# Kernel optimization log

Measured on AMD Instinct MI355X. Metric: run time of the kernel, lower is better.

Reference implementation:

```python
import jax, jax.numpy as jnp
import numpy as np

MAX_WORDS = 128  # static word capacity (stands in for dynamic max_word_num)


def setup_inputs() -> dict:
    key = jax.random.key(0)
    k1, k2 = jax.random.split(key)
    L, B, D = 512, 256, 256
    char_feats = jax.random.normal(k1, (L, B, D), dtype=jnp.float32)
    # sorted random word ids, densified so each row's ids are contiguous 0..n-1
    raw = jnp.sort(jax.random.randint(k2, (B, L), 0, MAX_WORDS), axis=1)
    bump = jnp.concatenate(
        [jnp.zeros((B, 1), jnp.int32), (raw[:, 1:] != raw[:, :-1]).astype(jnp.int32)],
        axis=1,
    )
    word_ids = jnp.cumsum(bump, axis=1)  # [B, L], non-decreasing, < MAX_WORDS
    attention_mask = jnp.ones((B, L), dtype=jnp.int32)
    return {"char_feats": char_feats, "word_ids": word_ids, "attention_mask": attention_mask}


def _pool(char_feats, word_ids, attention_mask):
    # char_feats: [L, B, D] time-major; word_ids/attention_mask: [B, L]
    L, B, D = char_feats.shape
    char_nums = jnp.sum(attention_mask, axis=1) - 2  # drop [CLS]/[SEP]
    pos = jnp.arange(L)
    # chars at positions 1 .. char_nums (inclusive) participate, per torch slicing
    valid = (pos[None, :] >= 1) & (pos[None, :] < 1 + char_nums[:, None])  # [B, L]
    seg = jnp.where(valid, word_ids, MAX_WORDS)  # overflow bucket for invalid chars
    feats_bld = jnp.transpose(char_feats, (1, 0, 2))  # [B, L, D]

    seg_sum = jax.vmap(
        lambda s, f: jax.ops.segment_sum(f, s, num_segments=MAX_WORDS + 1)
    )(seg, feats_bld)[:, :MAX_WORDS]  # [B, W, D]
    counts = jax.vmap(
        lambda s: jax.ops.segment_sum(jnp.ones((L,), jnp.float32), s, num_segments=MAX_WORDS + 1)
    )(seg)[:, :MAX_WORDS]  # [B, W]

    word_nums = jnp.max(word_ids, axis=1) + 1  # [B]
    masks = jnp.arange(MAX_WORDS)[:, None] < word_nums[None, :]  # [W, B]
    means = seg_sum / jnp.maximum(counts, 1.0)[..., None]  # counts>=1 within word_num
    word_feats = jnp.where(masks.T[..., None], means, 0.0)  # zero padded word slots
    return jnp.transpose(word_feats, (1, 0, 2)), masks  # [W, B, D], [W, B]


def reference(char_feats, word_ids, attention_mask):
    return _pool(char_feats, word_ids, attention_mask)
```

## Files before the change

kernel.cpp:

```cpp
#include <hip/hip_runtime.h>
#include <hip/hip_bf16.h>

#define LSEQ 512
#define BATCH 256
#define DIM 256
#define WMAX 128
#define WPB 16
#define BLOCKS_PER_B (WMAX / WPB)
#define ROW4 (BATCH * DIM / 4)
#define BD4 (DIM / 4)

__global__ __launch_bounds__(256) void word_pool_kernel(
    const float* __restrict__ feats,
    const int* __restrict__ word_ids,
    const int* __restrict__ amask,
    float* __restrict__ out)
{
    const int b = blockIdx.x >> 3;
    const int wbase = (blockIdx.x & 7) * WPB;
    const int t = threadIdx.x;

    __shared__ int sids[LSEQ];
    __shared__ int scount[WMAX];
    __shared__ int scum[WMAX];
    __shared__ int sstart[WMAX];
    __shared__ int s_masksum;

    if (t == 0) s_masksum = 0;
    if (t < WMAX) scount[t] = 0;
    __syncthreads();

    int msum = 0;
    for (int p = t; p < LSEQ; p += 256) {
        sids[p] = word_ids[b * LSEQ + p];
        msum += amask[b * LSEQ + p];
    }
    atomicAdd(&s_masksum, msum);
    __syncthreads();

    const int char_num = s_masksum - 2;
    const int word_num = sids[LSEQ - 1] + 1;
    int pend = 1 + char_num;
    if (pend > LSEQ) pend = LSEQ;

    for (int p = 1 + t; p < pend; p += 256) {
        atomicAdd(&scount[sids[p]], 1);
    }
    __syncthreads();

    if (t < WMAX) scum[t] = scount[t];
    __syncthreads();
    #pragma unroll
    for (int off = 1; off < WMAX; off <<= 1) {
        int add = 0;
        if (t < WMAX && t >= off) add = scum[t - off];
        __syncthreads();
        if (t < WMAX) scum[t] += add;
        __syncthreads();
    }
    if (t < WMAX) sstart[t] = 1 + (t > 0 ? scum[t - 1] : 0);
    __syncthreads();

    const int lane = t & 63;
    const int wi = t >> 6;
    const float4* __restrict__ f4 = (const float4*)feats;
    float4* __restrict__ o4 = (float4*)out;
    const int boff = b * BD4 + lane;

    for (int w = wbase + wi; w < wbase + WPB; w += 4) {
        const int c = scount[w];
        const int base = sstart[w];
        float4 acc = make_float4(0.f, 0.f, 0.f, 0.f);
        #pragma unroll 4
        for (int i = 0; i < c; i++) {
            float4 v = f4[(size_t)(base + i) * ROW4 + boff];
            acc.x += v.x; acc.y += v.y; acc.z += v.z; acc.w += v.w;
        }
        const float inv = 1.0f / (float)(c > 0 ? c : 1);
        float4 val = make_float4(acc.x * inv, acc.y * inv, acc.z * inv, acc.w * inv);
        o4[(size_t)w * ROW4 + boff] = val;
    }

    if (wbase == 0 && t < WMAX) {
        out[(size_t)WMAX * BATCH * DIM + (size_t)t * BATCH + b] =
            (t < word_num) ? 1.0f : 0.0f;
    }
}

extern "C" void kernel_launch(void* const* d_in, const int* in_sizes, int n_in,
                              void* d_out, int out_size, void* d_ws, size_t ws_size,
                              hipStream_t stream) {
    const float* char_feats = (const float*)d_in[0];
    const int* word_ids     = (const int*)d_in[1];
    const int* amask        = (const int*)d_in[2];
    float* out              = (float*)d_out;

    word_pool_kernel<<<BATCH * BLOCKS_PER_B, 256, 0, stream>>>(
        char_feats, word_ids, amask, out);
}
```

Before: 210.4 us.

## Balance word pooling by splitting character positions evenly across wavefronts

Instead of assigning a fixed 16 words per block and 4 words per wavefront, each block takes an equal slice of character positions and each wavefront a quarter of it. The wavefront then streams its rows and emits a word's mean whenever a boundary is crossed, so load balance no longer depends on word lengths. Word start positions now come from boundary detection on sorted ids, replacing the atomic histogram and shared-memory scan. Loads are software-pipelined in groups of four rows, and the id and mask reads use int4 plus a shuffle reduction. The trade-off is more complex control flow, with data-dependent branches inside the inner loop.

```diff
diff --git a/kernel.cpp b/kernel.cpp
--- a/kernel.cpp
+++ b/kernel.cpp
@@ -5,8 +5,7 @@
 #define BATCH 256
 #define DIM 256
 #define WMAX 128
-#define WPB 16
-#define BLOCKS_PER_B (WMAX / WPB)
+#define NCHUNK 8
 #define ROW4 (BATCH * DIM / 4)
 #define BD4 (DIM / 4)
 
@@ -17,71 +16,112 @@
     float* __restrict__ out)
 {
     const int b = blockIdx.x >> 3;
-    const int wbase = (blockIdx.x & 7) * WPB;
+    const int chunk = blockIdx.x & 7;
     const int t = threadIdx.x;
+    const int lane = t & 63;
+    const int wi = t >> 6;
 
     __shared__ int sids[LSEQ];
-    __shared__ int scount[WMAX];
-    __shared__ int scum[WMAX];
-    __shared__ int sstart[WMAX];
-    __shared__ int s_masksum;
+    __shared__ int sstart[WMAX + 1];
+    __shared__ int spart[4];
 
-    if (t == 0) s_masksum = 0;
-    if (t < WMAX) scount[t] = 0;
+    int msum = 0;
+    if (t < 128) {
+        int4 q = ((const int4*)(word_ids + b * LSEQ))[t];
+        ((int4*)sids)[t] = q;
+    } else {
+        int4 m = ((const int4*)(amask + b * LSEQ))[t - 128];
+        msum = m.x + m.y + m.z + m.w;
+    }
+    #pragma unroll
+    for (int off = 32; off; off >>= 1) msum += __shfl_down(msum, off, 64);
+    if (lane == 0) spart[wi] = msum;
     __syncthreads();
 
-    int msum = 0;
-    for (int p = t; p < LSEQ; p += 256) {
-        sids[p] = word_ids[b * LSEQ + p];
-        msum += amask[b * LSEQ + p];
-    }
-    atomicAdd(&s_masksum, msum);
+    const int char_num = spart[0] + spart[1] + spart[2] + spart[3] - 2;
+    int pend = 1 + char_num;
+    if (pend < 1) pend = 1;
+    if (pend > LSEQ) pend = LSEQ;
+
+    if (t <= WMAX) sstart[t] = pend;
     __syncthreads();
 
-    const int char_num = s_masksum - 2;
-    const int word_num = sids[LSEQ - 1] + 1;
-    int pend = 1 + char_num;
-    if (pend > LSEQ) pend = LSEQ;
-
     for (int p = 1 + t; p < pend; p += 256) {
-        atomicAdd(&scount[sids[p]], 1);
+        if (p == 1 || sids[p] != sids[p - 1]) sstart[sids[p]] = p;
     }
+    if (t == 0) sstart[0] = 1;
     __syncthreads();
 
-    if (t < WMAX) scum[t] = scount[t];
-    __syncthreads();
-    #pragma unroll
-    for (int off = 1; off < WMAX; off <<= 1) {
-        int add = 0;
-        if (t < WMAX && t >= off) add = scum[t - off];
-        __syncthreads();
-        if (t < WMAX) scum[t] += add;
-        __syncthreads();
-    }
-    if (t < WMAX) sstart[t] = 1 + (t > 0 ? scum[t - 1] : 0);
-    __syncthreads();
+    auto word_at = [&](int pos) -> int {
+        if (pos >= pend) return sids[pend - 1] + 1;
+        int w = sids[pos];
+        return (sstart[w] >= pos) ? w : w + 1;
+    };
 
-    const int lane = t & 63;
-    const int wi = t >> 6;
+    const int pend1 = pend - 1;
+    const int P0 = 1 + (chunk * pend1) / NCHUNK;
+    const int P1 = 1 + ((chunk + 1) * pend1) / NCHUNK;
+    const int span = P1 - P0;
+    const int Q0 = P0 + (wi * span) / 4;
+    const int Q1 = P0 + ((wi + 1) * span) / 4;
+
+    int w0 = (chunk == 0 && wi == 0) ? 0 : word_at(Q0);
+    int w1 = (chunk == NCHUNK - 1 && wi == 3) ? WMAX : word_at(Q1);
+
     const float4* __restrict__ f4 = (const float4*)feats;
     float4* __restrict__ o4 = (float4*)out;
     const int boff = b * BD4 + lane;
 
-    for (int w = wbase + wi; w < wbase + WPB; w += 4) {
-        const int c = scount[w];
-        const int base = sstart[w];
-        float4 acc = make_float4(0.f, 0.f, 0.f, 0.f);
-        #pragma unroll 4
-        for (int i = 0; i < c; i++) {
-            float4 v = f4[(size_t)(base + i) * ROW4 + boff];
+    const int p_lo = sstart[w0];
+    const int p_hi = sstart[w1];
+
+    int cur = w0;
+    int nxt = (cur < w1) ? sstart[cur + 1] : 0;
+    float4 acc = make_float4(0.f, 0.f, 0.f, 0.f);
+    int p = p_lo;
+
+    auto ldrow = [&](int r) -> float4 {
+        int rr = r < p_hi ? r : p_hi - 1;
+        return f4[(size_t)rr * ROW4 + boff];
+    };
+
+    float4 va0, va1, va2, va3;
+    if (p < p_hi) { va0 = ldrow(p); va1 = ldrow(p+1); va2 = ldrow(p+2); va3 = ldrow(p+3); }
+
+    while (p < p_hi) {
+        float4 vb0, vb1, vb2, vb3;
+        if (p + 4 < p_hi) { vb0 = ldrow(p+4); vb1 = ldrow(p+5); vb2 = ldrow(p+6); vb3 = ldrow(p+7); }
+        #pragma unroll
+        for (int j = 0; j < 4; j++) {
+            int pp = p + j;
+            if (pp >= p_hi) break;
+            while (pp >= nxt) {
+                int c = nxt - sstart[cur];
+                float inv = 1.0f / (float)(c > 0 ? c : 1);
+                o4[(size_t)cur * ROW4 + boff] =
+                    make_float4(acc.x * inv, acc.y * inv, acc.z * inv, acc.w * inv);
+                acc = make_float4(0.f, 0.f, 0.f, 0.f);
+                cur++;
+                nxt = sstart[cur + 1];
+            }
+            float4 v = (j == 0) ? va0 : (j == 1) ? va1 : (j == 2) ? va2 : va3;
             acc.x += v.x; acc.y += v.y; acc.z += v.z; acc.w += v.w;
         }
-        const float inv = 1.0f / (float)(c > 0 ? c : 1);
-        float4 val = make_float4(acc.x * inv, acc.y * inv, acc.z * inv, acc.w * inv);
-        o4[(size_t)w * ROW4 + boff] = val;
+        va0 = vb0; va1 = vb1; va2 = vb2; va3 = vb3;
+        p += 4;
     }
 
-    if (wbase == 0 && t < WMAX) {
+    while (cur < w1) {
+        int c = sstart[cur + 1] - sstart[cur];
+        float inv = 1.0f / (float)(c > 0 ? c : 1);
+        o4[(size_t)cur * ROW4 + boff] =
+            make_float4(acc.x * inv, acc.y * inv, acc.z * inv, acc.w * inv);
+        acc = make_float4(0.f, 0.f, 0.f, 0.f);
+        cur++;
+    }
+
+    if (chunk == 0 && t < WMAX) {
+        int word_num = sids[LSEQ - 1] + 1;
         out[(size_t)WMAX * BATCH * DIM + (size_t)t * BATCH + b] =
             (t < word_num) ? 1.0f : 0.0f;
     }
@@ -95,6 +135,6 @@
     const int* amask        = (const int*)d_in[2];
     float* out              = (float*)d_out;
 
-    word_pool_kernel<<<BATCH * BLOCKS_PER_B, 256, 0, stream>>>(
+    word_pool_kernel<<<BATCH * NCHUNK, 256, 0, stream>>>(
         char_feats, word_ids, amask, out);
 }
```

Result: no change. 207.9 us (-1.2%).

## Split segment metadata into separate kernel and batch feature loads in pool kernel

Applied to the files above, without the earlier changes.

Moves the per-batch word-boundary computation into a small meta kernel that finds segment starts by detecting id changes, replacing the atomic histogram and prefix scan. Word starts go to workspace, and a separate pool kernel gives each wavefront one word and issues up to eight loads at once before accumulating. The aim is to drop the metadata work that each of the eight blocks per batch repeated, and to raise memory-level parallelism in the reduction. The cost is a second launch and a round trip through workspace memory.

```diff
diff --git a/kernel.cpp b/kernel.cpp
--- a/kernel.cpp
+++ b/kernel.cpp
@@ -5,86 +5,99 @@
 #define BATCH 256
 #define DIM 256
 #define WMAX 128
-#define WPB 16
-#define BLOCKS_PER_B (WMAX / WPB)
 #define ROW4 (BATCH * DIM / 4)
 #define BD4 (DIM / 4)
+#define MSTRIDE (WMAX + 2)
 
-__global__ __launch_bounds__(256) void word_pool_kernel(
-    const float* __restrict__ feats,
+__global__ __launch_bounds__(256) void meta_kernel(
     const int* __restrict__ word_ids,
     const int* __restrict__ amask,
+    int* __restrict__ meta,
     float* __restrict__ out)
 {
-    const int b = blockIdx.x >> 3;
-    const int wbase = (blockIdx.x & 7) * WPB;
+    const int b = blockIdx.x;
     const int t = threadIdx.x;
+    const int lane = t & 63;
+    const int wi = t >> 6;
 
     __shared__ int sids[LSEQ];
-    __shared__ int scount[WMAX];
-    __shared__ int scum[WMAX];
-    __shared__ int sstart[WMAX];
-    __shared__ int s_masksum;
+    __shared__ int spart[4];
+    __shared__ int sstart[WMAX + 1];
 
-    if (t == 0) s_masksum = 0;
-    if (t < WMAX) scount[t] = 0;
+    int msum = 0;
+    if (t < 128) {
+        ((int4*)sids)[t] = ((const int4*)(word_ids + b * LSEQ))[t];
+    } else {
+        int4 m = ((const int4*)(amask + b * LSEQ))[t - 128];
+        msum = m.x + m.y + m.z + m.w;
+    }
+    #pragma unroll
+    for (int off = 32; off; off >>= 1) msum += __shfl_down(msum, off, 64);
+    if (lane == 0) spart[wi] = msum;
     __syncthreads();
 
-    int msum = 0;
-    for (int p = t; p < LSEQ; p += 256) {
-        sids[p] = word_ids[b * LSEQ + p];
-        msum += amask[b * LSEQ + p];
-    }
-    atomicAdd(&s_masksum, msum);
+    const int char_num = spart[0] + spart[1] + spart[2] + spart[3] - 2;
+    int pend = 1 + char_num;
+    if (pend < 1) pend = 1;
+    if (pend > LSEQ) pend = LSEQ;
+
+    if (t <= WMAX) sstart[t] = pend;
     __syncthreads();
 
-    const int char_num = s_masksum - 2;
-    const int word_num = sids[LSEQ - 1] + 1;
-    int pend = 1 + char_num;
-    if (pend > LSEQ) pend = LSEQ;
-
     for (int p = 1 + t; p < pend; p += 256) {
-        atomicAdd(&scount[sids[p]], 1);
+        if (p == 1 || sids[p] != sids[p - 1]) sstart[sids[p]] = p;
     }
+    if (t == 0) sstart[0] = 1;
     __syncthreads();
 
-    if (t < WMAX) scum[t] = scount[t];
-    __syncthreads();
-    #pragma unroll
-    for (int off = 1; off < WMAX; off <<= 1) {
-        int add = 0;
-        if (t < WMAX && t >= off) add = scum[t - off];
-        __syncthreads();
-        if (t < WMAX) scum[t] += add;
-        __syncthreads();
-    }
-    if (t < WMAX) sstart[t] = 1 + (t > 0 ? scum[t - 1] : 0);
-    __syncthreads();
+    if (t <= WMAX) meta[b * MSTRIDE + t] = sstart[t];
 
-    const int lane = t & 63;
-    const int wi = t >> 6;
-    const float4* __restrict__ f4 = (const float4*)feats;
-    float4* __restrict__ o4 = (float4*)out;
-    const int boff = b * BD4 + lane;
-
-    for (int w = wbase + wi; w < wbase + WPB; w += 4) {
-        const int c = scount[w];
-        const int base = sstart[w];
-        float4 acc = make_float4(0.f, 0.f, 0.f, 0.f);
-        #pragma unroll 4
-        for (int i = 0; i < c; i++) {
-            float4 v = f4[(size_t)(base + i) * ROW4 + boff];
-            acc.x += v.x; acc.y += v.y; acc.z += v.z; acc.w += v.w;
-        }
-        const float inv = 1.0f / (float)(c > 0 ? c : 1);
-        float4 val = make_float4(acc.x * inv, acc.y * inv, acc.z * inv, acc.w * inv);
-        o4[(size_t)w * ROW4 + boff] = val;
-    }
-
-    if (wbase == 0 && t < WMAX) {
+    if (t < WMAX) {
+        int word_num = sids[LSEQ - 1] + 1;
         out[(size_t)WMAX * BATCH * DIM + (size_t)t * BATCH + b] =
             (t < word_num) ? 1.0f : 0.0f;
     }
+}
+
+__global__ __launch_bounds__(256) void pool_kernel(
+    const float* __restrict__ feats,
+    const int* __restrict__ meta,
+    float* __restrict__ out)
+{
+    const int b = blockIdx.x >> 5;
+    const int wg = blockIdx.x & 31;
+    const int t = threadIdx.x;
+    const int lane = t & 63;
+    const int w = wg * 4 + (t >> 6);
+
+    const int* m = meta + b * MSTRIDE;
+    const int s0 = m[w];
+    const int s1 = m[w + 1];
+    const int c = s1 - s0;
+
+    const float4* __restrict__ f4 = (const float4*)feats;
+    const int boff = b * BD4 + lane;
+
+    float4 acc = make_float4(0.f, 0.f, 0.f, 0.f);
+    for (int i = 0; i < c; i += 8) {
+        const int n = c - i;
+        float4 v[8];
+        #pragma unroll
+        for (int j = 0; j < 8; j++) {
+            if (j < n) v[j] = f4[(size_t)(s0 + i + j) * ROW4 + boff];
+        }
+        #pragma unroll
+        for (int j = 0; j < 8; j++) {
+            if (j < n) {
+                acc.x += v[j].x; acc.y += v[j].y;
+                acc.z += v[j].z; acc.w += v[j].w;
+            }
+        }
+    }
+
+    const float inv = 1.0f / (float)(c > 0 ? c : 1);
+    ((float4*)out)[(size_t)w * ROW4 + boff] =
+        make_float4(acc.x * inv, acc.y * inv, acc.z * inv, acc.w * inv);
 }
 
 extern "C" void kernel_launch(void* const* d_in, const int* in_sizes, int n_in,
@@ -94,7 +107,8 @@
     const int* word_ids     = (const int*)d_in[1];
     const int* amask        = (const int*)d_in[2];
     float* out              = (float*)d_out;
+    int* meta               = (int*)d_ws;
 
-    word_pool_kernel<<<BATCH * BLOCKS_PER_B, 256, 0, stream>>>(
-        char_feats, word_ids, amask, out);
+    meta_kernel<<<BATCH, 256, 0, stream>>>(word_ids, amask, meta, out);
+    pool_kernel<<<BATCH * 32, 256, 0, stream>>>(char_feats, meta, out);
 }
```

Result: no change. 207.2 us (-1.5%).
